# Performance work log

Measured on AMD Instinct MI355X. Metric: run time of the kernel, lower is better.

Reference implementation:

```python
import jax, jax.numpy as jnp
import numpy as np

IN_, OUT_, HID, B = 1024, 1024, 4, 8192

def setup_inputs() -> dict:
    key = jax.random.key(0)
    k_x, k_w1, k_b1, k_w2, k_b2 = jax.random.split(key, 5)
    x = jax.random.normal(k_x, (B, IN_), dtype=jnp.float32)
    # Stacked params for out_ tiny MLPs: Linear(in,4) -> LeakyReLU(0.1) -> Linear(4,1)
    s1 = 1.0 / np.sqrt(IN_)
    s2 = 1.0 / np.sqrt(HID)
    W1 = jax.random.uniform(k_w1, (OUT_, IN_, HID), dtype=jnp.float32, minval=-s1, maxval=s1)
    b1 = jax.random.uniform(k_b1, (OUT_, HID), dtype=jnp.float32, minval=-s1, maxval=s1)
    W2 = jax.random.uniform(k_w2, (OUT_, HID), dtype=jnp.float32, minval=-s2, maxval=s2)
    b2 = jax.random.uniform(k_b2, (OUT_,), dtype=jnp.float32, minval=-s2, maxval=s2)
    return {"x": x, "W1": W1, "b1": b1, "W2": W2, "b2": b2}

def reference(x, W1, b1, W2, b2):
    # h[b,o,h] = x[b,:] @ W1[o] + b1[o]  (shared input across all out_ MLPs)
    h = jnp.einsum('bi,oih->boh', x, W1) + b1
    h = jnp.where(h >= 0, h, 0.1 * h)  # LeakyReLU(0.1)
    # out[b,o] = h[b,o,:] @ W2[o] + b2[o]; equals torch.cat of per-MLP scalars
    out = jnp.einsum('boh,oh->bo', h, W2) + b2
    return out
```

## Files before the change

kernel.cpp:

```cpp
#include <hip/hip_runtime.h>
#include <hip/hip_bf16.h>

#define IN_DIM  1024
#define OUT_DIM 1024
#define HID     4
#define BATCH   8192
#define NCOL    (OUT_DIM * HID)

typedef __bf16 bf16x8 __attribute__((ext_vector_type(8)));
typedef float  f32x4  __attribute__((ext_vector_type(4)));

__device__ __forceinline__ unsigned short f2bf(float f) {
  union { float f; unsigned int u; } v; v.f = f;
  unsigned int u = v.u;
  u += 0x7FFFu + ((u >> 16) & 1u);
  return (unsigned short)(u >> 16);
}

__global__ __launch_bounds__(256) void cvt_all_kernel(const float* __restrict__ x,
                                                      uint4* __restrict__ xg,
                                                      const float* __restrict__ W1,
                                                      ushort4* __restrict__ w1t) {
  int blk = blockIdx.x;
  if (blk < 4096) {
    int g = blk * 256 + threadIdx.x;
    int bl = g & 15, ko = (g >> 4) & 127, c4 = g >> 11;
    const float4* xp = (const float4*)(x + (size_t)(c4 * 16 + bl) * 1024 + ko * 8);
    float4 v0 = xp[0], v1 = xp[1];
    uint4 r;
    r.x = f2bf(v0.x) | ((unsigned)f2bf(v0.y) << 16);
    r.y = f2bf(v0.z) | ((unsigned)f2bf(v0.w) << 16);
    r.z = f2bf(v1.x) | ((unsigned)f2bf(v1.y) << 16);
    r.w = f2bf(v1.z) | ((unsigned)f2bf(v1.w) << 16);
    xg[g] = r;
  } else {
    int b = blk - 4096;
    int g = ((b & 7) * 512 + (b >> 3)) * 256 + threadIdx.x;
    int i4 = g & 255;
    int oh = g >> 8;
    int h = oh & 3, o = oh >> 2;
    const float* src = W1 + (size_t)o * 4096 + h;
    ushort4 r;
    r.x = f2bf(src[(i4 * 4 + 0) * 4]);
    r.y = f2bf(src[(i4 * 4 + 1) * 4]);
    r.z = f2bf(src[(i4 * 4 + 2) * 4]);
    r.w = f2bf(src[(i4 * 4 + 3) * 4]);
    w1t[(size_t)oh * 256 + i4] = r;
  }
}

__device__ __forceinline__ void gload16(const void* g, void* l) {
  __builtin_amdgcn_global_load_lds(
      (const __attribute__((address_space(1))) unsigned int*)g,
      (__attribute__((address_space(3))) unsigned int*)l, 16, 0, 0);
}

__global__ __launch_bounds__(256, 4) void mlp_gemm_kernel(
    const unsigned short* __restrict__ A,
    const unsigned short* __restrict__ Bg,
    const f32x4* __restrict__ b1v,
    const f32x4* __restrict__ w2v,
    const float* __restrict__ b2,
    float* __restrict__ out) {
  __shared__ __align__(16) unsigned short lds[16384];

  const int bid = blockIdx.x;
  const int xcd = bid & 7, loc = bid >> 3;
  const int bn = xcd * 8 + (loc & 7);
  const int bm = loc >> 3;
  const int tileM = bm * 128, tileN = bn * 128;

  const int t = threadIdx.x;
  const int lane = t & 63, wn = t >> 6;
  const int frow = lane & 15, jq = lane >> 4;

  const int sr8 = t >> 3, slt = t & 7;
  const int scol = ((slt ^ (sr8 & 7)) << 3);
  const unsigned short* Asrc = A + (size_t)(tileM + sr8) * IN_DIM + scol;

  auto stage = [&](int kt, int p) {
    const int kb = kt * 64;
    unsigned short* lA = lds + p * 8192 + t * 8;
#pragma unroll
    for (int i = 0; i < 4; ++i)
      gload16(Asrc + (size_t)(32 * i) * IN_DIM + kb, lA + i * 2048);
  };

  const int c40 = (tileN >> 4) + wn * 2;
  const char* bpB = (const char*)Bg + (((size_t)c40 * 128 + jq) * 16 + frow) * 16;

  f32x4 acc[8][2];
#pragma unroll
  for (int m = 0; m < 8; ++m) {
    acc[m][0] = f32x4{0.f, 0.f, 0.f, 0.f};
    acc[m][1] = f32x4{0.f, 0.f, 0.f, 0.f};
  }

  const int pk0 = (jq ^ (frow & 7)) << 3;
  const int pk1 = pk0 ^ 32;

  stage(0, 0);
  asm volatile("s_waitcnt vmcnt(0)" ::: "memory");
  __builtin_amdgcn_s_barrier();

  for (int kt = 0; kt < 16; ++kt) {
    const int cur = kt & 1;
    if (kt < 15) stage(kt + 1, cur ^ 1);

    const char* bk = bpB + kt * 2048;
    bf16x8 b00 = *(const bf16x8*)(bk);
    bf16x8 b01 = *(const bf16x8*)(bk + 1024);
    bf16x8 b10 = *(const bf16x8*)(bk + 32768);
    bf16x8 b11 = *(const bf16x8*)(bk + 32768 + 1024);

    const unsigned short* aB = lds + cur * 8192 + frow * 64;
    bf16x8 a[4];
#pragma unroll
    for (int i = 0; i < 4; ++i) a[i] = *(const bf16x8*)(aB + i * 1024 + pk0);
#pragma unroll
    for (int mf = 0; mf < 4; ++mf) {
      acc[mf][0] = __builtin_amdgcn_mfma_f32_16x16x32_bf16(a[mf], b00, acc[mf][0], 0, 0, 0);
      acc[mf][1] = __builtin_amdgcn_mfma_f32_16x16x32_bf16(a[mf], b10, acc[mf][1], 0, 0, 0);
    }
#pragma unroll
    for (int i = 0; i < 4; ++i) a[i] = *(const bf16x8*)(aB + (4 + i) * 1024 + pk0);
#pragma unroll
    for (int mf = 0; mf < 4; ++mf) {
      acc[4 + mf][0] = __builtin_amdgcn_mfma_f32_16x16x32_bf16(a[mf], b00, acc[4 + mf][0], 0, 0, 0);
      acc[4 + mf][1] = __builtin_amdgcn_mfma_f32_16x16x32_bf16(a[mf], b10, acc[4 + mf][1], 0, 0, 0);
    }
#pragma unroll
    for (int i = 0; i < 4; ++i) a[i] = *(const bf16x8*)(aB + i * 1024 + pk1);
#pragma unroll
    for (int mf = 0; mf < 4; ++mf) {
      acc[mf][0] = __builtin_amdgcn_mfma_f32_16x16x32_bf16(a[mf], b01, acc[mf][0], 0, 0, 0);
      acc[mf][1] = __builtin_amdgcn_mfma_f32_16x16x32_bf16(a[mf], b11, acc[mf][1], 0, 0, 0);
    }
#pragma unroll
    for (int i = 0; i < 4; ++i) a[i] = *(const bf16x8*)(aB + (4 + i) * 1024 + pk1);
#pragma unroll
    for (int mf = 0; mf < 4; ++mf) {
      acc[4 + mf][0] = __builtin_amdgcn_mfma_f32_16x16x32_bf16(a[mf], b01, acc[4 + mf][0], 0, 0, 0);
      acc[4 + mf][1] = __builtin_amdgcn_mfma_f32_16x16x32_bf16(a[mf], b11, acc[4 + mf][1], 0, 0, 0);
    }

    if (kt < 15) {
      asm volatile("s_waitcnt vmcnt(0)" ::: "memory");
      __builtin_amdgcn_s_barrier();
    }
  }
  __syncthreads();

  float* LE = (float*)lds;
  const int obase = tileM >> 2;
#pragma unroll
  for (int mf = 0; mf < 8; ++mf) {
    int o_loc = mf * 4 + jq;
    f32x4 b1q = b1v[obase + o_loc];
    f32x4 w2q = w2v[obase + o_loc];
#pragma unroll
    for (int nf = 0; nf < 2; ++nf) {
      int bat = wn * 32 + nf * 16 + frow;
      float v = 0.f;
#pragma unroll
      for (int h = 0; h < 4; ++h) {
        float hj = acc[mf][nf][h] + b1q[h];
        hj = (hj >= 0.f) ? hj : 0.1f * hj;
        v += hj * w2q[h];
      }
      LE[bat * 33 + o_loc] = v;
    }
  }
  __syncthreads();

  const int col = t & 31, rowb = t >> 5;
  const float b2s = b2[obase + col];
  float* outB = out + (size_t)tileN * OUT_DIM + obase;
#pragma unroll
  for (int i = 0; i < 16; ++i) {
    int row = rowb + i * 8;
    outB[(size_t)row * OUT_DIM + col] = LE[row * 33 + col] + b2s;
  }
}

__global__ __launch_bounds__(256) void fallback_kernel(
    const float* __restrict__ x, const float* __restrict__ W1,
    const float* __restrict__ b1, const float* __restrict__ W2,
    const float* __restrict__ b2, float* __restrict__ out) {
  int idx = blockIdx.x * 256 + threadIdx.x;
  if (idx >= BATCH * OUT_DIM) return;
  int bb = idx >> 10, o = idx & 1023;
  const float4* w1p = (const float4*)(W1 + (size_t)o * 4096);
  const float*  xp  = x + (size_t)bb * 1024;
  float4 acc = *(const float4*)(b1 + o * 4);
  for (int i = 0; i < 1024; ++i) {
    float xv = xp[i];
    float4 w = w1p[i];
    acc.x += xv * w.x; acc.y += xv * w.y; acc.z += xv * w.z; acc.w += xv * w.w;
  }
  float4 w2 = *(const float4*)(W2 + o * 4);
  float r = b2[o];
  r += ((acc.x >= 0.f) ? acc.x : 0.1f * acc.x) * w2.x;
  r += ((acc.y >= 0.f) ? acc.y : 0.1f * acc.y) * w2.y;
  r += ((acc.z >= 0.f) ? acc.z : 0.1f * acc.z) * w2.z;
  r += ((acc.w >= 0.f) ? acc.w : 0.1f * acc.w) * w2.w;
  out[(size_t)bb * OUT_DIM + o] = r;
}

extern "C" void kernel_launch(void* const* d_in, const int* in_sizes, int n_in,
                              void* d_out, int out_size, void* d_ws, size_t ws_size,
                              hipStream_t stream) {
  const float* x  = (const float*)d_in[0];
  const float* W1 = (const float*)d_in[1];
  const float* b1 = (const float*)d_in[2];
  const float* W2 = (const float*)d_in[3];
  const float* b2 = (const float*)d_in[4];
  float* out = (float*)d_out;

  size_t need = (size_t)BATCH * IN_DIM * 2 + (size_t)NCOL * IN_DIM * 2;
  if (ws_size >= need) {
    unsigned short* xg  = (unsigned short*)d_ws;
    unsigned short* w1t = xg + (size_t)BATCH * IN_DIM;
    cvt_all_kernel<<<8192, 256, 0, stream>>>(x, (uint4*)xg, W1, (ushort4*)w1t);
    mlp_gemm_kernel<<<(NCOL / 128) * (BATCH / 128), 256, 0, stream>>>(
        w1t, xg, (const f32x4*)b1, (const f32x4*)W2, b2, out);
  } else {
    fallback_kernel<<<(BATCH * OUT_DIM + 255) / 256, 256, 0, stream>>>(x, W1, b1, W2, b2, out);
  }
}
```

Baseline: 81.99 us.

## Switch GEMM wave layout from 1x4 to 2x2 warp tiling

Each of the four waves now computes a 64x64 sub-tile (2x2 wave grid) instead of a 128x32 strip. Per K step a wave does half the LDS A-fragment reads while loading twice as many B fragments straight from global memory, which cuts LDS traffic per MFMA. The occupancy hint drops from 4 to 3 blocks per CU, which allows more registers for the larger B-fragment set but leaves fewer resident waves to hide latency.

Measured after the change: 86.13 us. 5.1% more time.

```diff
diff --git a/kernel.cpp b/kernel.cpp
--- a/kernel.cpp
+++ b/kernel.cpp
@@ -55,7 +55,7 @@
       (__attribute__((address_space(3))) unsigned int*)l, 16, 0, 0);
 }
 
-__global__ __launch_bounds__(256, 4) void mlp_gemm_kernel(
+__global__ __launch_bounds__(256, 3) void mlp_gemm_kernel(
     const unsigned short* __restrict__ A,
     const unsigned short* __restrict__ Bg,
     const f32x4* __restrict__ b1v,
@@ -71,7 +71,8 @@
   const int tileM = bm * 128, tileN = bn * 128;
 
   const int t = threadIdx.x;
-  const int lane = t & 63, wn = t >> 6;
+  const int lane = t & 63, wid = t >> 6;
+  const int wm = wid >> 1, wn = wid & 1;
   const int frow = lane & 15, jq = lane >> 4;
 
   const int sr8 = t >> 3, slt = t & 7;
@@ -86,18 +87,18 @@
       gload16(Asrc + (size_t)(32 * i) * IN_DIM + kb, lA + i * 2048);
   };
 
-  const int c40 = (tileN >> 4) + wn * 2;
+  const int c40 = (tileN >> 4) + wn * 4;
   const char* bpB = (const char*)Bg + (((size_t)c40 * 128 + jq) * 16 + frow) * 16;
 
-  f32x4 acc[8][2];
-#pragma unroll
-  for (int m = 0; m < 8; ++m) {
-    acc[m][0] = f32x4{0.f, 0.f, 0.f, 0.f};
-    acc[m][1] = f32x4{0.f, 0.f, 0.f, 0.f};
-  }
+  f32x4 acc[4][4];
+#pragma unroll
+  for (int m = 0; m < 4; ++m)
+#pragma unroll
+    for (int n = 0; n < 4; ++n) acc[m][n] = f32x4{0.f, 0.f, 0.f, 0.f};
 
   const int pk0 = (jq ^ (frow & 7)) << 3;
   const int pk1 = pk0 ^ 32;
+  const int aOff = wm * 4096 + frow * 64;
 
   stage(0, 0);
   asm volatile("s_waitcnt vmcnt(0)" ::: "memory");
@@ -108,41 +109,29 @@
     if (kt < 15) stage(kt + 1, cur ^ 1);
 
     const char* bk = bpB + kt * 2048;
-    bf16x8 b00 = *(const bf16x8*)(bk);
-    bf16x8 b01 = *(const bf16x8*)(bk + 1024);
-    bf16x8 b10 = *(const bf16x8*)(bk + 32768);
-    bf16x8 b11 = *(const bf16x8*)(bk + 32768 + 1024);
-
-    const unsigned short* aB = lds + cur * 8192 + frow * 64;
+    bf16x8 b0[4], b1r[4];
+#pragma unroll
+    for (int nf = 0; nf < 4; ++nf) {
+      b0[nf]  = *(const bf16x8*)(bk + nf * 32768);
+      b1r[nf] = *(const bf16x8*)(bk + nf * 32768 + 1024);
+    }
+
+    const unsigned short* aB = lds + cur * 8192 + aOff;
     bf16x8 a[4];
 #pragma unroll
     for (int i = 0; i < 4; ++i) a[i] = *(const bf16x8*)(aB + i * 1024 + pk0);
 #pragma unroll
-    for (int mf = 0; mf < 4; ++mf) {
-      acc[mf][0] = __builtin_amdgcn_mfma_f32_16x16x32_bf16(a[mf], b00, acc[mf][0], 0, 0, 0);
-      acc[mf][1] = __builtin_amdgcn_mfma_f32_16x16x32_bf16(a[mf], b10, acc[mf][1], 0, 0, 0);
-    }
-#pragma unroll
-    for (int i = 0; i < 4; ++i) a[i] = *(const bf16x8*)(aB + (4 + i) * 1024 + pk0);
-#pragma unroll
-    for (int mf = 0; mf < 4; ++mf) {
-      acc[4 + mf][0] = __builtin_amdgcn_mfma_f32_16x16x32_bf16(a[mf], b00, acc[4 + mf][0], 0, 0, 0);
-      acc[4 + mf][1] = __builtin_amdgcn_mfma_f32_16x16x32_bf16(a[mf], b10, acc[4 + mf][1], 0, 0, 0);
-    }
+    for (int mf = 0; mf < 4; ++mf)
+#pragma unroll
+      for (int nf = 0; nf < 4; ++nf)
+        acc[mf][nf] = __builtin_amdgcn_mfma_f32_16x16x32_bf16(a[mf], b0[nf], acc[mf][nf], 0, 0, 0);
 #pragma unroll
     for (int i = 0; i < 4; ++i) a[i] = *(const bf16x8*)(aB + i * 1024 + pk1);
 #pragma unroll
-    for (int mf = 0; mf < 4; ++mf) {
-      acc[mf][0] = __builtin_amdgcn_mfma_f32_16x16x32_bf16(a[mf], b01, acc[mf][0], 0, 0, 0);
-      acc[mf][1] = __builtin_amdgcn_mfma_f32_16x16x32_bf16(a[mf], b11, acc[mf][1], 0, 0, 0);
-    }
-#pragma unroll
-    for (int i = 0; i < 4; ++i) a[i] = *(const bf16x8*)(aB + (4 + i) * 1024 + pk1);
-#pragma unroll
-    for (int mf = 0; mf < 4; ++mf) {
-      acc[4 + mf][0] = __builtin_amdgcn_mfma_f32_16x16x32_bf16(a[mf], b01, acc[4 + mf][0], 0, 0, 0);
-      acc[4 + mf][1] = __builtin_amdgcn_mfma_f32_16x16x32_bf16(a[mf], b11, acc[4 + mf][1], 0, 0, 0);
-    }
+    for (int mf = 0; mf < 4; ++mf)
+#pragma unroll
+      for (int nf = 0; nf < 4; ++nf)
+        acc[mf][nf] = __builtin_amdgcn_mfma_f32_16x16x32_bf16(a[mf], b1r[nf], acc[mf][nf], 0, 0, 0);
 
     if (kt < 15) {
       asm volatile("s_waitcnt vmcnt(0)" ::: "memory");
@@ -154,13 +143,13 @@
   float* LE = (float*)lds;
   const int obase = tileM >> 2;
 #pragma unroll
-  for (int mf = 0; mf < 8; ++mf) {
-    int o_loc = mf * 4 + jq;
+  for (int mf = 0; mf < 4; ++mf) {
+    int o_loc = wm * 16 + mf * 4 + jq;
     f32x4 b1q = b1v[obase + o_loc];
     f32x4 w2q = w2v[obase + o_loc];
 #pragma unroll
-    for (int nf = 0; nf < 2; ++nf) {
-      int bat = wn * 32 + nf * 16 + frow;
+    for (int nf = 0; nf < 4; ++nf) {
+      int bat = wn * 64 + nf * 16 + frow;
       float v = 0.f;
 #pragma unroll
       for (int h = 0; h < 4; ++h) {
```

## Triple-buffer LDS A tiles and double-buffer B register loads in GEMM loop

Applied to the files above, without the earlier changes.

Switches the main GEMM loop from a double-buffered LDS stage to a three-stage ring that prefetches two k-tiles ahead. B fragments are prefetched into alternating register sets one iteration early. A partial vmcnt wait replaces the full drain so one stage of loads can stay in flight. Scheduling barriers pin the instruction order. LDS grows to 48 KB and the occupancy hint drops from 4 to 3 blocks, and the loop is fully unrolled by hand.

Measured after the change: 83.19 us. No clear change (+1.5%).

```diff
diff --git a/kernel.cpp b/kernel.cpp
--- a/kernel.cpp
+++ b/kernel.cpp
@@ -55,14 +55,14 @@
       (__attribute__((address_space(3))) unsigned int*)l, 16, 0, 0);
 }
 
-__global__ __launch_bounds__(256, 4) void mlp_gemm_kernel(
+__global__ __launch_bounds__(256, 3) void mlp_gemm_kernel(
     const unsigned short* __restrict__ A,
     const unsigned short* __restrict__ Bg,
     const f32x4* __restrict__ b1v,
     const f32x4* __restrict__ w2v,
     const float* __restrict__ b2,
     float* __restrict__ out) {
-  __shared__ __align__(16) unsigned short lds[16384];
+  __shared__ __align__(16) unsigned short lds[24576];
 
   const int bid = blockIdx.x;
   const int xcd = bid & 7, loc = bid >> 3;
@@ -99,56 +99,80 @@
   const int pk0 = (jq ^ (frow & 7)) << 3;
   const int pk1 = pk0 ^ 32;
 
+  bf16x8 bA[4], bB[4];
+
+#define SB() __builtin_amdgcn_sched_barrier(0)
+
+#define LOADB(S, kt_) do {                                                     \
+    const char* bk_ = bpB + (kt_) * 2048;                                      \
+    S[0] = *(const bf16x8*)(bk_);                                              \
+    S[1] = *(const bf16x8*)(bk_ + 1024);                                       \
+    S[2] = *(const bf16x8*)(bk_ + 32768);                                      \
+    S[3] = *(const bf16x8*)(bk_ + 32768 + 1024);                               \
+  } while (0)
+
+#define KT(kt_, pr_, ps_, BC, BN_, mode_) do {                                 \
+    if (mode_ == 0) stage(kt_ + 2, ps_);                                       \
+    SB();                                            \
+    const unsigned short* aB_ = lds + (pr_) * 8192 + frow * 64;                \
+    bf16x8 a_[4];                                                              \
+    _Pragma("unroll")                                                          \
+    for (int i_ = 0; i_ < 4; ++i_) a_[i_] = *(const bf16x8*)(aB_ + i_ * 1024 + pk0); \
+    _Pragma("unroll")                                                          \
+    for (int mf_ = 0; mf_ < 4; ++mf_) {                                        \
+      acc[mf_][0] = __builtin_amdgcn_mfma_f32_16x16x32_bf16(a_[mf_], BC[0], acc[mf_][0], 0, 0, 0); \
+      acc[mf_][1] = __builtin_amdgcn_mfma_f32_16x16x32_bf16(a_[mf_], BC[2], acc[mf_][1], 0, 0, 0); \
+    }                                                                          \
+    _Pragma("unroll")                                                          \
+    for (int i_ = 0; i_ < 4; ++i_) a_[i_] = *(const bf16x8*)(aB_ + (4 + i_) * 1024 + pk0); \
+    _Pragma("unroll")                                                          \
+    for (int mf_ = 0; mf_ < 4; ++mf_) {                                        \
+      acc[4 + mf_][0] = __builtin_amdgcn_mfma_f32_16x16x32_bf16(a_[mf_], BC[0], acc[4 + mf_][0], 0, 0, 0); \
+      acc[4 + mf_][1] = __builtin_amdgcn_mfma_f32_16x16x32_bf16(a_[mf_], BC[2], acc[4 + mf_][1], 0, 0, 0); \
+    }                                                                          \
+    _Pragma("unroll")                                                          \
+    for (int i_ = 0; i_ < 4; ++i_) a_[i_] = *(const bf16x8*)(aB_ + i_ * 1024 + pk1); \
+    _Pragma("unroll")                                                          \
+    for (int mf_ = 0; mf_ < 4; ++mf_) {                                        \
+      acc[mf_][0] = __builtin_amdgcn_mfma_f32_16x16x32_bf16(a_[mf_], BC[1], acc[mf_][0], 0, 0, 0); \
+      acc[mf_][1] = __builtin_amdgcn_mfma_f32_16x16x32_bf16(a_[mf_], BC[3], acc[mf_][1], 0, 0, 0); \
+    }                                                                          \
+    _Pragma("unroll")                                                          \
+    for (int i_ = 0; i_ < 4; ++i_) a_[i_] = *(const bf16x8*)(aB_ + (4 + i_) * 1024 + pk1); \
+    _Pragma("unroll")                                                          \
+    for (int mf_ = 0; mf_ < 4; ++mf_) {                                        \
+      acc[4 + mf_][0] = __builtin_amdgcn_mfma_f32_16x16x32_bf16(a_[mf_], BC[1], acc[4 + mf_][0], 0, 0, 0); \
+      acc[4 + mf_][1] = __builtin_amdgcn_mfma_f32_16x16x32_bf16(a_[mf_], BC[3], acc[4 + mf_][1], 0, 0, 0); \
+    }                                                                          \
+    if (mode_ <= 1) {                                                          \
+      SB();                                        \
+      LOADB(BN_, kt_ + 1);                                                     \
+      SB();                                                  \
+      if (mode_ == 0) asm volatile("s_waitcnt vmcnt(8)" ::: "memory");         \
+      else            asm volatile("s_waitcnt vmcnt(0)" ::: "memory");         \
+      __builtin_amdgcn_s_barrier();                                            \
+    }                                                                          \
+  } while (0)
+
   stage(0, 0);
-  asm volatile("s_waitcnt vmcnt(0)" ::: "memory");
+  SB();
+  stage(1, 1);
+  SB();
+  LOADB(bA, 0);
+  SB();
+  asm volatile("s_waitcnt vmcnt(8)" ::: "memory");
   __builtin_amdgcn_s_barrier();
 
-  for (int kt = 0; kt < 16; ++kt) {
-    const int cur = kt & 1;
-    if (kt < 15) stage(kt + 1, cur ^ 1);
-
-    const char* bk = bpB + kt * 2048;
-    bf16x8 b00 = *(const bf16x8*)(bk);
-    bf16x8 b01 = *(const bf16x8*)(bk + 1024);
-    bf16x8 b10 = *(const bf16x8*)(bk + 32768);
-    bf16x8 b11 = *(const bf16x8*)(bk + 32768 + 1024);
-
-    const unsigned short* aB = lds + cur * 8192 + frow * 64;
-    bf16x8 a[4];
-#pragma unroll
-    for (int i = 0; i < 4; ++i) a[i] = *(const bf16x8*)(aB + i * 1024 + pk0);
-#pragma unroll
-    for (int mf = 0; mf < 4; ++mf) {
-      acc[mf][0] = __builtin_amdgcn_mfma_f32_16x16x32_bf16(a[mf], b00, acc[mf][0], 0, 0, 0);
-      acc[mf][1] = __builtin_amdgcn_mfma_f32_16x16x32_bf16(a[mf], b10, acc[mf][1], 0, 0, 0);
-    }
-#pragma unroll
-    for (int i = 0; i < 4; ++i) a[i] = *(const bf16x8*)(aB + (4 + i) * 1024 + pk0);
-#pragma unroll
-    for (int mf = 0; mf < 4; ++mf) {
-      acc[4 + mf][0] = __builtin_amdgcn_mfma_f32_16x16x32_bf16(a[mf], b00, acc[4 + mf][0], 0, 0, 0);
-      acc[4 + mf][1] = __builtin_amdgcn_mfma_f32_16x16x32_bf16(a[mf], b10, acc[4 + mf][1], 0, 0, 0);
-    }
-#pragma unroll
-    for (int i = 0; i < 4; ++i) a[i] = *(const bf16x8*)(aB + i * 1024 + pk1);
-#pragma unroll
-    for (int mf = 0; mf < 4; ++mf) {
-      acc[mf][0] = __builtin_amdgcn_mfma_f32_16x16x32_bf16(a[mf], b01, acc[mf][0], 0, 0, 0);
-      acc[mf][1] = __builtin_amdgcn_mfma_f32_16x16x32_bf16(a[mf], b11, acc[mf][1], 0, 0, 0);
-    }
-#pragma unroll
-    for (int i = 0; i < 4; ++i) a[i] = *(const bf16x8*)(aB + (4 + i) * 1024 + pk1);
-#pragma unroll
-    for (int mf = 0; mf < 4; ++mf) {
-      acc[4 + mf][0] = __builtin_amdgcn_mfma_f32_16x16x32_bf16(a[mf], b01, acc[4 + mf][0], 0, 0, 0);
-      acc[4 + mf][1] = __builtin_amdgcn_mfma_f32_16x16x32_bf16(a[mf], b11, acc[4 + mf][1], 0, 0, 0);
-    }
-
-    if (kt < 15) {
-      asm volatile("s_waitcnt vmcnt(0)" ::: "memory");
-      __builtin_amdgcn_s_barrier();
-    }
-  }
+  KT( 0, 0, 2, bA, bB, 0); KT( 1, 1, 0, bB, bA, 0); KT( 2, 2, 1, bA, bB, 0);
+  KT( 3, 0, 2, bB, bA, 0); KT( 4, 1, 0, bA, bB, 0); KT( 5, 2, 1, bB, bA, 0);
+  KT( 6, 0, 2, bA, bB, 0); KT( 7, 1, 0, bB, bA, 0); KT( 8, 2, 1, bA, bB, 0);
+  KT( 9, 0, 2, bB, bA, 0); KT(10, 1, 0, bA, bB, 0); KT(11, 2, 1, bB, bA, 0);
+  KT(12, 0, 2, bA, bB, 0); KT(13, 1, 0, bB, bA, 0);
+  KT(14, 2, 0, bA, bB, 1);
+  KT(15, 0, 0, bB, bA, 2);
+#undef KT
+#undef LOADB
+#undef SB
   __syncthreads();
 
   float* LE = (float*)lds;
```
